# Kernel tuning notes

Measured on AMD Instinct MI355X. Metric: run time of the kernel, lower is better.

Reference implementation:

```python
import jax, jax.numpy as jnp
import numpy as np

B, N, M = 2, 2048, 2048
Q_DIM = 1024
HEADS = 8
DIM_HEAD = 64
INNER = HEADS * DIM_HEAD  # 512


def setup_inputs() -> dict:
    key = jax.random.key(0)
    ks = jax.random.split(key, 7)
    s_in = 1.0 / np.sqrt(Q_DIM)
    s_out = 1.0 / np.sqrt(INNER)
    return {
        "x": jax.random.normal(ks[0], (B, N, Q_DIM), dtype=jnp.float32),
        "context": jax.random.normal(ks[1], (B, M, Q_DIM), dtype=jnp.float32),
        "Wq": jax.random.normal(ks[2], (Q_DIM, INNER), dtype=jnp.float32) * s_in,
        "Wk": jax.random.normal(ks[3], (Q_DIM, INNER), dtype=jnp.float32) * s_in,
        "Wv": jax.random.normal(ks[4], (Q_DIM, INNER), dtype=jnp.float32) * s_in,
        "Wo": jax.random.normal(ks[5], (INNER, Q_DIM), dtype=jnp.float32) * s_out,
        "bo": jax.random.normal(ks[6], (Q_DIM,), dtype=jnp.float32) * 0.01,
    }


def reference(x, context, Wq, Wk, Wv, Wo, bo):
    scale = DIM_HEAD ** (-0.5)
    # projections, split heads: [b, n, inner] -> [b, h, n, d]
    def split_heads(t):
        b, n, _ = t.shape
        return t.reshape(b, n, HEADS, DIM_HEAD).transpose(0, 2, 1, 3)
    q = split_heads(x @ Wq)
    k = split_heads(context @ Wk)
    v = split_heads(context @ Wv)
    sim = jnp.einsum('bhid,bhjd->bhij', q, k) * scale  # [b,h,n,m] full score matrix
    attn = jax.nn.softmax(sim, axis=-1)
    out = jnp.einsum('bhij,bhjd->bhid', attn, v)       # [b,h,n,d]
    out = out.transpose(0, 2, 1, 3).reshape(x.shape[0], x.shape[1], INNER)
    return out @ Wo + bo
```

## Files before the change

kernel.cpp:

```cpp
#include <hip/hip_runtime.h>

typedef __attribute__((ext_vector_type(8))) short short8;
typedef __attribute__((ext_vector_type(4))) float floatx4;
typedef __attribute__((ext_vector_type(16))) float f32x16;
typedef __attribute__((ext_vector_type(4))) float f32x4;
typedef __attribute__((ext_vector_type(2))) unsigned uint2v;

__device__ __forceinline__ short f2bf(float f) {
    union { float f; unsigned u; } v;
    v.f = f;
    unsigned r = v.u + 0x7fffu + ((v.u >> 16) & 1u);
    return (short)(r >> 16);
}

#define MFMA_BF16(a, b, c) __builtin_amdgcn_mfma_f32_16x16x32_bf16((a), (b), (c), 0, 0, 0)
#define MFMA32(a, b, c)    __builtin_amdgcn_mfma_f32_32x32x16_bf16((a), (b), (c), 0, 0, 0)

__device__ __forceinline__ float fast_exp2(float x) {
#if __has_builtin(__builtin_amdgcn_exp2f)
    return __builtin_amdgcn_exp2f(x);
#else
    return exp2f(x);
#endif
}

__device__ __forceinline__ unsigned cvtpk(float lo, float hi) {
    unsigned r;
    asm("v_cvt_pk_bf16_f32 %0, %1, %2" : "=v"(r) : "v"(lo), "v"(hi));
    return r;
}

__device__ __forceinline__ void pl32(unsigned& a, unsigned& b) {
    asm("v_permlane32_swap_b32 %0, %1" : "+v"(a), "+v"(b));
}

__device__ __forceinline__ void gll16(const void* g, void* l) {
    __builtin_amdgcn_global_load_lds((const __attribute__((address_space(1))) void*)g,
                                     (__attribute__((address_space(3))) void*)l,
                                     16, 0, 0);
}

#define QSCALE_LOG2E 0.18033688011112042f

__global__ __launch_bounds__(256) void wfrag_all(const float* __restrict__ Wq,
                                                 const float* __restrict__ Wk,
                                                 const float* __restrict__ Wv,
                                                 const float* __restrict__ Wo,
                                                 short* __restrict__ WqF,
                                                 short* __restrict__ WkF,
                                                 short* __restrict__ WvF,
                                                 short* __restrict__ WoF) {
    const int z = blockIdx.y;
    const float* src = (z == 0) ? Wq : (z == 1) ? Wk : (z == 2) ? Wv : Wo;
    short* dst = (z == 0) ? WqF : (z == 1) ? WkF : (z == 2) ? WvF : WoF;
    const int nbits = (z < 3) ? 9 : 10;
    const int N = 1 << nbits;
    const int t = blockIdx.x * 256 + threadIdx.x;
    const int kb = t >> nbits;
    const int n = t & (N - 1);
    const float* s = src + (size_t)(kb * 8) * N + n;
    short8 v;
#pragma unroll
    for (int j = 0; j < 8; ++j) v[j] = f2bf(s[(size_t)j * N]);
    *(short8*)(dst + (size_t)t * 8) = v;
}

__global__ __launch_bounds__(256) void afrag(const float* __restrict__ x,
                                             const float* __restrict__ ctx,
                                             short* __restrict__ AxF,
                                             short* __restrict__ AcF) {
    const float* src = (blockIdx.z == 0) ? x : ctx;
    short* dst = (blockIdx.z == 0) ? AxF : AcF;
    const int r0 = blockIdx.x * 64;
    const int k0 = blockIdx.y * 64;
    __shared__ short tile[64][72];
    const int tid = threadIdx.x;
    {
        const int seg = tid & 15;
        const int rbase = tid >> 4;
#pragma unroll
        for (int i = 0; i < 4; ++i) {
            const int row = rbase + i * 16;
            f32x4 v = *(const f32x4*)(src + (size_t)(r0 + row) * 1024 + k0 + seg * 4);
            uint2v d;
            d[0] = cvtpk(v[0], v[1]);
            d[1] = cvtpk(v[2], v[3]);
            *(uint2v*)&tile[row][seg * 4] = d;
        }
    }
    __syncthreads();
    {
        const int kbl = tid >> 5;
        const int rbase = tid & 31;
#pragma unroll
        for (int j = 0; j < 2; ++j) {
            const int row = rbase + j * 32;
            short8 v = *(const short8*)(&tile[row][kbl * 8]);
            *(short8*)(dst + ((size_t)(k0 / 8 + kbl) * 4096 + r0 + row) * 8) = v;
        }
    }
}

__global__ __launch_bounds__(256) void gemm_qkv(const short* __restrict__ AxF,
                                                const short* __restrict__ AcF,
                                                const short* __restrict__ WqF,
                                                const short* __restrict__ WkF,
                                                const short* __restrict__ WvF,
                                                short* __restrict__ Qw,
                                                short* __restrict__ Kw,
                                                short* __restrict__ Vtw) {
    const int z = blockIdx.z;
    const short* AF = (z == 0) ? AxF : AcF;
    const short* WF = (z == 0) ? WqF : (z == 1) ? WkF : WvF;
    const int tid = threadIdx.x;
    const int w = tid >> 6;
    const int lane = tid & 63;
    const int quad = lane >> 4, ln = lane & 15;
    const int wr = w >> 1, wc = w & 1;
    const int row0 = blockIdx.x * 64;
    const int col0 = blockIdx.y * 128;

    __shared__ __align__(16) short lds[2][12288];

    auto stage = [&](int buf, int kt) {
        short* d = &lds[buf][0];
        const int kb0 = kt * 8;
#pragma unroll
        for (int c = 0; c < 2; ++c) {
            const int kb = c * 4 + w;
            gll16(AF + ((size_t)(kb0 + kb) * 4096 + row0 + lane) * 8,
                  d + kb * 512);
        }
#pragma unroll
        for (int c = 0; c < 4; ++c) {
            const int g = c * 4 + w;
            const int kb = g >> 1, colb = (g & 1) * 64;
            gll16(WF + ((size_t)(kb0 + kb) * 512 + col0 + colb + lane) * 8,
                  d + 4096 + (kb * 128 + colb) * 8);
        }
    };

    floatx4 acc[2][4] = {};

    auto compute = [&](int buf) {
        const short* sA = &lds[buf][0];
        const short* sB = &lds[buf][4096];
#pragma unroll
        for (int s = 0; s < 2; ++s) {
            const int kb = s * 4 + quad;
            short8 aF[2], bF[4];
#pragma unroll
            for (int i = 0; i < 2; ++i)
                aF[i] = *(const short8*)(sA + (kb * 64 + wr * 32 + i * 16 + ln) * 8);
#pragma unroll
            for (int j = 0; j < 4; ++j)
                bF[j] = *(const short8*)(sB + (kb * 128 + wc * 64 + j * 16 + ln) * 8);
#pragma unroll
            for (int i = 0; i < 2; ++i)
#pragma unroll
                for (int j = 0; j < 4; ++j)
                    acc[i][j] = MFMA_BF16(aF[i], bF[j], acc[i][j]);
        }
    };

    stage(0, 0);
    __syncthreads();
    for (int t = 0; t < 16; ++t) {
        if (t + 1 < 16) stage((t + 1) & 1, t + 1);
        compute(t & 1);
        __syncthreads();
    }

    const float oscale = (z == 0) ? QSCALE_LOG2E : 1.0f;
    short* dst = (z == 0) ? Qw : (z == 1) ? Kw : Vtw;
#pragma unroll
    for (int i = 0; i < 2; ++i)
#pragma unroll
        for (int t = 0; t < 4; ++t)
#pragma unroll
            for (int r = 0; r < 4; ++r) {
                const int R = row0 + wr * 32 + i * 16 + quad * 4 + r;
                const int C = col0 + wc * 64 + t * 16 + ln;
                const int b = R >> 11, n = R & 2047;
                const int h = C >> 6, d = C & 63;
                const short val = f2bf(acc[i][t][r] * oscale);
                if (z < 2)
                    dst[((b * 8 + h) * 2048 + n) * 64 + d] = val;
                else
                    dst[((b * 8 + h) * 64 + d) * 2048 + n] = val;
            }
}

__global__ __launch_bounds__(256, 2) void attn_kernel(const short* __restrict__ Q,
                                                      const short* __restrict__ K,
                                                      const short* __restrict__ Vt,
                                                      short* __restrict__ AwF) {
    const int tid = threadIdx.x;
    const int w = tid >> 6;
    const int lane = tid & 63;
    const int hi = lane >> 5;
    const int ln5 = lane & 31;

    const int L = blockIdx.x + 32 * blockIdx.y;
    const int xcd = L & 7, slot = L >> 3;
    const int bh = xcd * 2 + (slot >> 5);
    const int q0 = (slot & 31) * 64;

    __shared__ __align__(16) char smem[65536];
    char* const wbase = smem + w * 16384;

    const short* Qbh = Q + (size_t)bh * 2048 * 64;
    const char* kp = (const char*)(K + (size_t)bh * 2048 * 64);
    const char* vp = (const char*)(Vt + (size_t)bh * 64 * 2048);

    short8 qf[2][4];
#pragma unroll
    for (int qt = 0; qt < 2; ++qt)
#pragma unroll
        for (int ds = 0; ds < 4; ++ds)
            qf[qt][ds] = *(const short8*)(Qbh + (size_t)(q0 + qt * 32 + ln5) * 64 + ds * 16 + hi * 8);

    f32x16 O[2][2] = {};
    float lp0 = 0.f, lp1 = 0.f;

    const int lrow = lane >> 3, lu = lane & 7;
    const int swzK = ((lu ^ lrow) << 4);
    const int sw_r = (ln5 & 7) << 4;

    auto stageK = [&](int tile, int c) {
        char* kb = wbase + c * 8192;
#pragma unroll
        for (int i = 0; i < 4; ++i)
            gll16(kp + (size_t)tile * 4096 + (size_t)i * 1024 + lrow * 128 + swzK,
                  kb + i * 1024);
    };
    auto stageV = [&](int tile, int c) {
        char* vb = wbase + c * 8192 + 4096;
#pragma unroll
        for (int i = 0; i < 4; ++i) {
            const int u = lu ^ lrow;
            const int d = i * 8 + lrow + 32 * (u >> 2);
            gll16(vp + (size_t)d * 4096 + (size_t)tile * 64 + (u & 3) * 16,
                  vb + i * 1024);
        }
    };

    short8 PA[2][2];

    auto computeTile = [&](int c) {
        char* kb = wbase + c * 8192;
        char* vb = kb + 4096;
        short8 kf[4];
#pragma unroll
        for (int ds = 0; ds < 4; ++ds)
            kf[ds] = *(const short8*)(kb + ln5 * 128 + ((((ds * 2 + hi) << 4)) ^ sw_r));
        short8 vf[2][2];
#pragma unroll
        for (int dt = 0; dt < 2; ++dt)
#pragma unroll
            for (int k2 = 0; k2 < 2; ++k2)
                vf[dt][k2] = *(const short8*)(vb + ln5 * 128 +
                                              ((((dt * 4 + k2 * 2 + hi) << 4)) ^ sw_r));
        f32x16 s0 = {}, s1 = {};
        __builtin_amdgcn_s_setprio(1);
#pragma unroll
        for (int ds = 0; ds < 4; ++ds) {
            s0 = MFMA32(kf[ds], qf[0][ds], s0);
            s1 = MFMA32(kf[ds], qf[1][ds], s1);
        }
        __builtin_amdgcn_s_setprio(0);
        auto buildPA = [&](const f32x16& sv, float& lacc, short8& oA, short8& oB) {
            float p[16];
#pragma unroll
            for (int e = 0; e < 16; ++e) p[e] = fast_exp2(sv[e]);
            float t0 = 0.f, t1 = 0.f;
#pragma unroll
            for (int e = 0; e < 16; e += 2) { t0 += p[e]; t1 += p[e + 1]; }
            lacc += t0 + t1;
            unsigned c0 = cvtpk(p[0], p[1]),   c1 = cvtpk(p[2], p[3]);
            unsigned c2 = cvtpk(p[4], p[5]),   c3 = cvtpk(p[6], p[7]);
            unsigned c4 = cvtpk(p[8], p[9]),   c5 = cvtpk(p[10], p[11]);
            unsigned c6 = cvtpk(p[12], p[13]), c7 = cvtpk(p[14], p[15]);
            pl32(c0, c2); pl32(c1, c3);
            pl32(c4, c6); pl32(c5, c7);
            union U { short8 s8; unsigned u[4]; };
            U a; a.u[0] = c0; a.u[1] = c1; a.u[2] = c2; a.u[3] = c3; oA = a.s8;
            U b; b.u[0] = c4; b.u[1] = c5; b.u[2] = c6; b.u[3] = c7; oB = b.s8;
        };
        buildPA(s0, lp0, PA[0][0], PA[1][0]);
        buildPA(s1, lp1, PA[0][1], PA[1][1]);
        __builtin_amdgcn_s_setprio(1);
#pragma unroll
        for (int dt = 0; dt < 2; ++dt)
#pragma unroll
            for (int k2 = 0; k2 < 2; ++k2) {
                O[dt][0] = MFMA32(vf[dt][k2], PA[k2][0], O[dt][0]);
                O[dt][1] = MFMA32(vf[dt][k2], PA[k2][1], O[dt][1]);
            }
        __builtin_amdgcn_s_setprio(0);
    };

    stageK(w, 0);
    stageV(w, 0);
    int cur = 0;
    for (int t = 0; t < 16; ++t) {
        if (t < 15) {
            stageK(w + (t + 1) * 4, cur ^ 1);
            stageV(w + (t + 1) * 4, cur ^ 1);
            asm volatile("s_waitcnt vmcnt(8)" ::: "memory");
        } else {
            asm volatile("s_waitcnt vmcnt(0)" ::: "memory");
        }
        computeTile(cur);
        cur ^= 1;
    }
    __syncthreads();

    float* lpf = (float*)smem;
    {
        const float a = lp0 + __shfl_xor(lp0, 32);
        const float b = lp1 + __shfl_xor(lp1, 32);
        if (hi == 0) {
            lpf[w * 64 + ln5] = a;
            lpf[w * 64 + 32 + ln5] = b;
        }
    }
    __syncthreads();
    const int qq = tid & 63;
    const int k8a = tid >> 6;
    const float den = lpf[qq] + lpf[64 + qq] + lpf[128 + qq] + lpf[192 + qq];
    const float inv = 1.0f / den;
    __syncthreads();
    float* freg = (float*)smem + w * 4096;
#pragma unroll
    for (int dt = 0; dt < 2; ++dt)
#pragma unroll
        for (int qt = 0; qt < 2; ++qt)
#pragma unroll
            for (int e = 0; e < 16; ++e) {
                const int d = dt * 32 + (e & 3) + 8 * (e >> 2) + 4 * hi;
                freg[d * 64 + qt * 32 + ln5] = O[dt][qt][e];
            }
    __syncthreads();
    const int b = bh >> 3, h = bh & 7;
    const float* fall = (const float*)smem;
#pragma unroll
    for (int j = 0; j < 2; ++j) {
        const int k8 = k8a + j * 4;
        float a8[8];
#pragma unroll
        for (int dd = 0; dd < 8; ++dd) {
            const int d = k8 * 8 + dd;
            a8[dd] = fall[d * 64 + qq] + fall[4096 + d * 64 + qq] +
                     fall[8192 + d * 64 + qq] + fall[12288 + d * 64 + qq];
        }
        short8 o8;
#pragma unroll
        for (int dd = 0; dd < 8; ++dd) o8[dd] = f2bf(a8[dd] * inv);
        *(short8*)(AwF + ((size_t)(h * 8 + k8) * 4096 + (size_t)(b * 2048 + q0 + qq)) * 8) = o8;
    }
}

__global__ __launch_bounds__(256) void gemm_final(const short* __restrict__ AwF,
                                                  const short* __restrict__ WoF,
                                                  const float* __restrict__ bias,
                                                  float* __restrict__ out) {
    const int tid = threadIdx.x;
    const int w = tid >> 6;
    const int lane = tid & 63;
    const int quad = lane >> 4, ln = lane & 15;
    const int wr = w >> 1, wc = w & 1;
    const int row0 = blockIdx.x * 64;
    const int col0 = blockIdx.y * 128;

    __shared__ __align__(16) short lds[2][12288];

    auto stage = [&](int buf, int kt) {
        short* d = &lds[buf][0];
        const int kb0 = kt * 8;
#pragma unroll
        for (int c = 0; c < 2; ++c) {
            const int kb = c * 4 + w;
            gll16(AwF + ((size_t)(kb0 + kb) * 4096 + row0 + lane) * 8,
                  d + kb * 512);
        }
#pragma unroll
        for (int c = 0; c < 4; ++c) {
            const int g = c * 4 + w;
            const int kb = g >> 1, colb = (g & 1) * 64;
            gll16(WoF + ((size_t)(kb0 + kb) * 1024 + col0 + colb + lane) * 8,
                  d + 4096 + (kb * 128 + colb) * 8);
        }
    };

    floatx4 acc[2][4] = {};

    auto compute = [&](int buf) {
        const short* sA = &lds[buf][0];
        const short* sB = &lds[buf][4096];
#pragma unroll
        for (int s = 0; s < 2; ++s) {
            const int kb = s * 4 + quad;
            short8 aF[2], bF[4];
#pragma unroll
            for (int i = 0; i < 2; ++i)
                aF[i] = *(const short8*)(sA + (kb * 64 + wr * 32 + i * 16 + ln) * 8);
#pragma unroll
            for (int j = 0; j < 4; ++j)
                bF[j] = *(const short8*)(sB + (kb * 128 + wc * 64 + j * 16 + ln) * 8);
#pragma unroll
            for (int i = 0; i < 2; ++i)
#pragma unroll
                for (int j = 0; j < 4; ++j)
                    acc[i][j] = MFMA_BF16(aF[i], bF[j], acc[i][j]);
        }
    };

    stage(0, 0);
    __syncthreads();
    for (int t = 0; t < 8; ++t) {
        if (t + 1 < 8) stage((t + 1) & 1, t + 1);
        compute(t & 1);
        __syncthreads();
    }

#pragma unroll
    for (int i = 0; i < 2; ++i)
#pragma unroll
        for (int t = 0; t < 4; ++t)
#pragma unroll
            for (int r = 0; r < 4; ++r) {
                const int R = row0 + wr * 32 + i * 16 + quad * 4 + r;
                const int C = col0 + wc * 64 + t * 16 + ln;
                out[(size_t)R * 1024 + C] = acc[i][t][r] + bias[C];
            }
}

extern "C" void kernel_launch(void* const* d_in, const int* in_sizes, int n_in,
                              void* d_out, int out_size, void* d_ws, size_t ws_size,
                              hipStream_t stream) {
    const float* x   = (const float*)d_in[0];
    const float* ctx = (const float*)d_in[1];
    const float* Wq  = (const float*)d_in[2];
    const float* Wk  = (const float*)d_in[3];
    const float* Wv  = (const float*)d_in[4];
    const float* Wo  = (const float*)d_in[5];
    const float* bo  = (const float*)d_in[6];
    float* out = (float*)d_out;

    char* ws = (char*)d_ws;
    size_t off = 0;
    auto alloc = [&](size_t bytes) { char* p = ws + off; off += (bytes + 255) & ~(size_t)255; return p; };

    short* WqF  = (short*)alloc(512 * 1024 * 2);
    short* WkF  = (short*)alloc(512 * 1024 * 2);
    short* WvF  = (short*)alloc(512 * 1024 * 2);
    short* WoF  = (short*)alloc(1024 * 512 * 2);
    short* AxF  = (short*)alloc((size_t)4096 * 1024 * 2);
    short* AcF  = (short*)alloc((size_t)4096 * 1024 * 2);
    short* Qw   = (short*)alloc((size_t)16 * 2048 * 64 * 2);
    short* Kw   = (short*)alloc((size_t)16 * 2048 * 64 * 2);
    short* Vtw  = (short*)alloc((size_t)16 * 2048 * 64 * 2);
    short* AwF  = (short*)alloc((size_t)4096 * 512 * 2);

    wfrag_all<<<dim3(256, 4), 256, 0, stream>>>(Wq, Wk, Wv, Wo, WqF, WkF, WvF, WoF);
    afrag<<<dim3(64, 16, 2), 256, 0, stream>>>(x, ctx, AxF, AcF);

    gemm_qkv<<<dim3(64, 4, 3), 256, 0, stream>>>(AxF, AcF, WqF, WkF, WvF, Qw, Kw, Vtw);

    attn_kernel<<<dim3(32, 16), 256, 0, stream>>>(Qw, Kw, Vtw, AwF);

    gemm_final<<<dim3(64, 8), 256, 0, stream>>>(AwF, WoF, bo, out);
}
```

Measured before the change: 150.1 us.

## Stage V-transpose through LDS and double attention block query tile

The QKV GEMM epilogue for V now transposes the tile in shared memory and writes Vt with 16-byte vector stores instead of scattered 2-byte strided stores. The attention kernel moves to 512-thread blocks covering 128 queries: two query halves share the same per-wave K/V split, 128KB of LDS, and half as many blocks. This is meant to cut uncoalesced global writes and raise K/V reuse per block. In exchange it lowers block count (256 blocks at one per CU) and doubles the LDS footprint.

```diff
diff --git a/kernel.cpp b/kernel.cpp
--- a/kernel.cpp
+++ b/kernel.cpp
@@ -172,26 +172,47 @@
     }
 
     const float oscale = (z == 0) ? QSCALE_LOG2E : 1.0f;
-    short* dst = (z == 0) ? Qw : (z == 1) ? Kw : Vtw;
-#pragma unroll
-    for (int i = 0; i < 2; ++i)
-#pragma unroll
-        for (int t = 0; t < 4; ++t)
-#pragma unroll
-            for (int r = 0; r < 4; ++r) {
-                const int R = row0 + wr * 32 + i * 16 + quad * 4 + r;
-                const int C = col0 + wc * 64 + t * 16 + ln;
-                const int b = R >> 11, n = R & 2047;
-                const int h = C >> 6, d = C & 63;
-                const short val = f2bf(acc[i][t][r] * oscale);
-                if (z < 2)
-                    dst[((b * 8 + h) * 2048 + n) * 64 + d] = val;
-                else
-                    dst[((b * 8 + h) * 64 + d) * 2048 + n] = val;
-            }
-}
-
-__global__ __launch_bounds__(256, 2) void attn_kernel(const short* __restrict__ Q,
+    if (z < 2) {
+        short* dst = (z == 0) ? Qw : Kw;
+#pragma unroll
+        for (int i = 0; i < 2; ++i)
+#pragma unroll
+            for (int t = 0; t < 4; ++t)
+#pragma unroll
+                for (int r = 0; r < 4; ++r) {
+                    const int R = row0 + wr * 32 + i * 16 + quad * 4 + r;
+                    const int C = col0 + wc * 64 + t * 16 + ln;
+                    const int b = R >> 11, n = R & 2047;
+                    const int h = C >> 6, d = C & 63;
+                    dst[((b * 8 + h) * 2048 + n) * 64 + d] = f2bf(acc[i][t][r] * oscale);
+                }
+    } else {
+        short* t2 = (short*)&lds[0][0];
+#pragma unroll
+        for (int i = 0; i < 2; ++i)
+#pragma unroll
+            for (int t = 0; t < 4; ++t)
+#pragma unroll
+                for (int r = 0; r < 4; ++r) {
+                    const int lr = wr * 32 + i * 16 + quad * 4 + r;
+                    const int lc = wc * 64 + t * 16 + ln;
+                    t2[lc * 72 + lr] = f2bf(acc[i][t][r]);
+                }
+        __syncthreads();
+        const int c = tid >> 1, halfr = (tid & 1) * 32;
+        const int C = col0 + c;
+        const int h = C >> 6, d = C & 63;
+        const int b = row0 >> 11;
+        const int n0 = (row0 & 2047) + halfr;
+        short* gp = Vtw + (((size_t)(b * 8 + h) * 64 + d) * 2048) + n0;
+        const short* sp = t2 + c * 72 + halfr;
+#pragma unroll
+        for (int u = 0; u < 4; ++u)
+            *(short8*)(gp + u * 8) = *(const short8*)(sp + u * 8);
+    }
+}
+
+__global__ __launch_bounds__(512, 1) void attn_kernel(const short* __restrict__ Q,
                                                       const short* __restrict__ K,
                                                       const short* __restrict__ Vt,
                                                       short* __restrict__ AwF) {
@@ -200,25 +221,28 @@
     const int lane = tid & 63;
     const int hi = lane >> 5;
     const int ln5 = lane & 31;
-
-    const int L = blockIdx.x + 32 * blockIdx.y;
+    const int qh = w & 1;
+    const int kvr = w >> 1;
+
+    const int L = blockIdx.x + 16 * blockIdx.y;
     const int xcd = L & 7, slot = L >> 3;
-    const int bh = xcd * 2 + (slot >> 5);
-    const int q0 = (slot & 31) * 64;
-
-    __shared__ __align__(16) char smem[65536];
+    const int bh = xcd * 2 + (slot >> 4);
+    const int q0 = (slot & 15) * 128;
+
+    __shared__ __align__(16) char smem[131072];
     char* const wbase = smem + w * 16384;
 
     const short* Qbh = Q + (size_t)bh * 2048 * 64;
     const char* kp = (const char*)(K + (size_t)bh * 2048 * 64);
     const char* vp = (const char*)(Vt + (size_t)bh * 64 * 2048);
 
+    const int qbase = q0 + qh * 64;
     short8 qf[2][4];
 #pragma unroll
     for (int qt = 0; qt < 2; ++qt)
 #pragma unroll
         for (int ds = 0; ds < 4; ++ds)
-            qf[qt][ds] = *(const short8*)(Qbh + (size_t)(q0 + qt * 32 + ln5) * 64 + ds * 16 + hi * 8);
+            qf[qt][ds] = *(const short8*)(Qbh + (size_t)(qbase + qt * 32 + ln5) * 64 + ds * 16 + hi * 8);
 
     f32x16 O[2][2] = {};
     float lp0 = 0.f, lp1 = 0.f;
@@ -300,13 +324,13 @@
         __builtin_amdgcn_s_setprio(0);
     };
 
-    stageK(w, 0);
-    stageV(w, 0);
+    stageK(kvr, 0);
+    stageV(kvr, 0);
     int cur = 0;
     for (int t = 0; t < 16; ++t) {
         if (t < 15) {
-            stageK(w + (t + 1) * 4, cur ^ 1);
-            stageV(w + (t + 1) * 4, cur ^ 1);
+            stageK(kvr + (t + 1) * 4, cur ^ 1);
+            stageV(kvr + (t + 1) * 4, cur ^ 1);
             asm volatile("s_waitcnt vmcnt(8)" ::: "memory");
         } else {
             asm volatile("s_waitcnt vmcnt(0)" ::: "memory");
@@ -321,14 +345,16 @@
         const float a = lp0 + __shfl_xor(lp0, 32);
         const float b = lp1 + __shfl_xor(lp1, 32);
         if (hi == 0) {
-            lpf[w * 64 + ln5] = a;
-            lpf[w * 64 + 32 + ln5] = b;
-        }
-    }
-    __syncthreads();
-    const int qq = tid & 63;
-    const int k8a = tid >> 6;
-    const float den = lpf[qq] + lpf[64 + qq] + lpf[128 + qq] + lpf[192 + qq];
+            lpf[(qh * 4 + kvr) * 64 + ln5] = a;
+            lpf[(qh * 4 + kvr) * 64 + 32 + ln5] = b;
+        }
+    }
+    __syncthreads();
+    const int qq = tid & 127;
+    const int k8a = tid >> 7;
+    const int g = qq >> 6, qr = qq & 63;
+    const float den = lpf[(g * 4 + 0) * 64 + qr] + lpf[(g * 4 + 1) * 64 + qr] +
+                      lpf[(g * 4 + 2) * 64 + qr] + lpf[(g * 4 + 3) * 64 + qr];
     const float inv = 1.0f / den;
     __syncthreads();
     float* freg = (float*)smem + w * 4096;
@@ -351,8 +377,8 @@
 #pragma unroll
         for (int dd = 0; dd < 8; ++dd) {
             const int d = k8 * 8 + dd;
-            a8[dd] = fall[d * 64 + qq] + fall[4096 + d * 64 + qq] +
-                     fall[8192 + d * 64 + qq] + fall[12288 + d * 64 + qq];
+            a8[dd] = fall[(g + 0) * 4096 + d * 64 + qr] + fall[(g + 2) * 4096 + d * 64 + qr] +
+                     fall[(g + 4) * 4096 + d * 64 + qr] + fall[(g + 6) * 4096 + d * 64 + qr];
         }
         short8 o8;
 #pragma unroll
@@ -468,7 +494,7 @@
 
     gemm_qkv<<<dim3(64, 4, 3), 256, 0, stream>>>(AxF, AcF, WqF, WkF, WvF, Qw, Kw, Vtw);
 
-    attn_kernel<<<dim3(32, 16), 256, 0, stream>>>(Qw, Kw, Vtw, AwF);
+    attn_kernel<<<dim3(16, 16), 512, 0, stream>>>(Qw, Kw, Vtw, AwF);
 
     gemm_final<<<dim3(64, 8), 256, 0, stream>>>(AwF, WoF, bo, out);
 }
```

New measurement: 152.5 us. No clear change (+1.6%).

## Fuse fp32-to-bf16 activation conversion into QKV GEMM and stage V transpose via LDS

Applied to the files above, without the earlier changes.

Removes the separate afrag kernel and its intermediate bf16 fragment buffers. The QKV GEMM now reads fp32 x/context directly, converts to bf16 in registers and writes a padded row-major A tile into LDS, with loads for the next tile issued before compute. The V output is transposed through LDS so each thread writes contiguous 16-byte vectors instead of strided scalar stores. The cost is that each GEMM block reads fp32 A data, twice the bytes of the old bf16 fragments, and A is re-read across column blocks and the K/V z-slices. Converting in registers also adds VALU work to the GEMM loop.

```diff
diff --git a/kernel.cpp b/kernel.cpp
--- a/kernel.cpp
+++ b/kernel.cpp
@@ -65,44 +65,8 @@
     *(short8*)(dst + (size_t)t * 8) = v;
 }
 
-__global__ __launch_bounds__(256) void afrag(const float* __restrict__ x,
-                                             const float* __restrict__ ctx,
-                                             short* __restrict__ AxF,
-                                             short* __restrict__ AcF) {
-    const float* src = (blockIdx.z == 0) ? x : ctx;
-    short* dst = (blockIdx.z == 0) ? AxF : AcF;
-    const int r0 = blockIdx.x * 64;
-    const int k0 = blockIdx.y * 64;
-    __shared__ short tile[64][72];
-    const int tid = threadIdx.x;
-    {
-        const int seg = tid & 15;
-        const int rbase = tid >> 4;
-#pragma unroll
-        for (int i = 0; i < 4; ++i) {
-            const int row = rbase + i * 16;
-            f32x4 v = *(const f32x4*)(src + (size_t)(r0 + row) * 1024 + k0 + seg * 4);
-            uint2v d;
-            d[0] = cvtpk(v[0], v[1]);
-            d[1] = cvtpk(v[2], v[3]);
-            *(uint2v*)&tile[row][seg * 4] = d;
-        }
-    }
-    __syncthreads();
-    {
-        const int kbl = tid >> 5;
-        const int rbase = tid & 31;
-#pragma unroll
-        for (int j = 0; j < 2; ++j) {
-            const int row = rbase + j * 32;
-            short8 v = *(const short8*)(&tile[row][kbl * 8]);
-            *(short8*)(dst + ((size_t)(k0 / 8 + kbl) * 4096 + r0 + row) * 8) = v;
-        }
-    }
-}
-
-__global__ __launch_bounds__(256) void gemm_qkv(const short* __restrict__ AxF,
-                                                const short* __restrict__ AcF,
+__global__ __launch_bounds__(256) void gemm_qkv(const float* __restrict__ x,
+                                                const float* __restrict__ ctx,
                                                 const short* __restrict__ WqF,
                                                 const short* __restrict__ WkF,
                                                 const short* __restrict__ WvF,
@@ -110,7 +74,7 @@
                                                 short* __restrict__ Kw,
                                                 short* __restrict__ Vtw) {
     const int z = blockIdx.z;
-    const short* AF = (z == 0) ? AxF : AcF;
+    const float* As = (z == 0) ? x : ctx;
     const short* WF = (z == 0) ? WqF : (z == 1) ? WkF : WvF;
     const int tid = threadIdx.x;
     const int w = tid >> 6;
@@ -120,38 +84,52 @@
     const int row0 = blockIdx.x * 64;
     const int col0 = blockIdx.y * 128;
 
-    __shared__ __align__(16) short lds[2][12288];
-
-    auto stage = [&](int buf, int kt) {
-        short* d = &lds[buf][0];
+    __shared__ __align__(16) short lds[25600];
+    auto aP = [&](int buf) { return lds + buf * 4608; };
+    auto bP = [&](int buf) { return lds + 9216 + buf * 8192; };
+
+    const int seg = tid & 15;
+    const int rb = tid >> 4;
+
+    auto loadA = [&](int kt, f32x4* vn) {
+#pragma unroll
+        for (int i = 0; i < 4; ++i)
+            vn[i] = *(const f32x4*)(As + (size_t)(row0 + rb + i * 16) * 1024 + kt * 64 + seg * 4);
+    };
+    auto writeA = [&](int buf, const f32x4* vn) {
+        short* a = aP(buf);
+#pragma unroll
+        for (int i = 0; i < 4; ++i) {
+            uint2v d;
+            d[0] = cvtpk(vn[i][0], vn[i][1]);
+            d[1] = cvtpk(vn[i][2], vn[i][3]);
+            *(uint2v*)(a + (rb + i * 16) * 72 + seg * 4) = d;
+        }
+    };
+    auto stageB = [&](int buf, int kt) {
+        short* d = bP(buf);
         const int kb0 = kt * 8;
-#pragma unroll
-        for (int c = 0; c < 2; ++c) {
-            const int kb = c * 4 + w;
-            gll16(AF + ((size_t)(kb0 + kb) * 4096 + row0 + lane) * 8,
-                  d + kb * 512);
-        }
 #pragma unroll
         for (int c = 0; c < 4; ++c) {
             const int g = c * 4 + w;
             const int kb = g >> 1, colb = (g & 1) * 64;
             gll16(WF + ((size_t)(kb0 + kb) * 512 + col0 + colb + lane) * 8,
-                  d + 4096 + (kb * 128 + colb) * 8);
+                  d + (kb * 128 + colb) * 8);
         }
     };
 
     floatx4 acc[2][4] = {};
 
     auto compute = [&](int buf) {
-        const short* sA = &lds[buf][0];
-        const short* sB = &lds[buf][4096];
+        const short* sA = aP(buf);
+        const short* sB = bP(buf);
 #pragma unroll
         for (int s = 0; s < 2; ++s) {
             const int kb = s * 4 + quad;
             short8 aF[2], bF[4];
 #pragma unroll
             for (int i = 0; i < 2; ++i)
-                aF[i] = *(const short8*)(sA + (kb * 64 + wr * 32 + i * 16 + ln) * 8);
+                aF[i] = *(const short8*)(sA + (wr * 32 + i * 16 + ln) * 72 + kb * 8);
 #pragma unroll
             for (int j = 0; j < 4; ++j)
                 bF[j] = *(const short8*)(sB + (kb * 128 + wc * 64 + j * 16 + ln) * 8);
@@ -163,32 +141,66 @@
         }
     };
 
-    stage(0, 0);
-    __syncthreads();
+    {
+        f32x4 v0[4];
+        loadA(0, v0);
+        stageB(0, 0);
+        writeA(0, v0);
+    }
+    __syncthreads();
+    int cur = 0;
     for (int t = 0; t < 16; ++t) {
-        if (t + 1 < 16) stage((t + 1) & 1, t + 1);
-        compute(t & 1);
+        f32x4 vn[4];
+        const bool more = (t + 1 < 16);
+        if (more) {
+            loadA(t + 1, vn);
+            stageB(cur ^ 1, t + 1);
+        }
+        compute(cur);
+        if (more) writeA(cur ^ 1, vn);
         __syncthreads();
+        cur ^= 1;
     }
 
     const float oscale = (z == 0) ? QSCALE_LOG2E : 1.0f;
-    short* dst = (z == 0) ? Qw : (z == 1) ? Kw : Vtw;
-#pragma unroll
-    for (int i = 0; i < 2; ++i)
-#pragma unroll
-        for (int t = 0; t < 4; ++t)
-#pragma unroll
-            for (int r = 0; r < 4; ++r) {
-                const int R = row0 + wr * 32 + i * 16 + quad * 4 + r;
-                const int C = col0 + wc * 64 + t * 16 + ln;
-                const int b = R >> 11, n = R & 2047;
-                const int h = C >> 6, d = C & 63;
-                const short val = f2bf(acc[i][t][r] * oscale);
-                if (z < 2)
-                    dst[((b * 8 + h) * 2048 + n) * 64 + d] = val;
-                else
-                    dst[((b * 8 + h) * 64 + d) * 2048 + n] = val;
-            }
+    if (z < 2) {
+        short* dst = (z == 0) ? Qw : Kw;
+#pragma unroll
+        for (int i = 0; i < 2; ++i)
+#pragma unroll
+            for (int t = 0; t < 4; ++t)
+#pragma unroll
+                for (int r = 0; r < 4; ++r) {
+                    const int R = row0 + wr * 32 + i * 16 + quad * 4 + r;
+                    const int C = col0 + wc * 64 + t * 16 + ln;
+                    const int b = R >> 11, n = R & 2047;
+                    const int h = C >> 6, d = C & 63;
+                    dst[((b * 8 + h) * 2048 + n) * 64 + d] = f2bf(acc[i][t][r] * oscale);
+                }
+    } else {
+        short* t2 = lds;
+#pragma unroll
+        for (int i = 0; i < 2; ++i)
+#pragma unroll
+            for (int t = 0; t < 4; ++t)
+#pragma unroll
+                for (int r = 0; r < 4; ++r) {
+                    const int lr = wr * 32 + i * 16 + quad * 4 + r;
+                    const int lc = wc * 64 + t * 16 + ln;
+                    t2[lc * 72 + lr] = f2bf(acc[i][t][r]);
+                }
+        __syncthreads();
+        const int c = tid >> 1, halfr = (tid & 1) * 32;
+        const int C = col0 + c;
+        const int h = C >> 6, d = C & 63;
+        const int b = row0 >> 11;
+        const int n0 = (row0 & 2047) + halfr;
+        short* gp = Vtw + (((size_t)(b * 8 + h) * 64 + d) * 2048) + n0;
+        const short* sp = t2 + c * 72 + halfr;
+#pragma unroll
+        for (int u = 0; u < 4; ++u)
+            *(short8*)(gp + u * 8) = *(const short8*)(sp + u * 8);
+    }
 }
 
 __global__ __launch_bounds__(256, 2) void attn_kernel(const short* __restrict__ Q,
@@ -456,17 +468,14 @@
     short* WkF  = (short*)alloc(512 * 1024 * 2);
     short* WvF  = (short*)alloc(512 * 1024 * 2);
     short* WoF  = (short*)alloc(1024 * 512 * 2);
-    short* AxF  = (short*)alloc((size_t)4096 * 1024 * 2);
-    short* AcF  = (short*)alloc((size_t)4096 * 1024 * 2);
     short* Qw   = (short*)alloc((size_t)16 * 2048 * 64 * 2);
     short* Kw   = (short*)alloc((size_t)16 * 2048 * 64 * 2);
     short* Vtw  = (short*)alloc((size_t)16 * 2048 * 64 * 2);
     short* AwF  = (short*)alloc((size_t)4096 * 512 * 2);
 
     wfrag_all<<<dim3(256, 4), 256, 0, stream>>>(Wq, Wk, Wv, Wo, WqF, WkF, WvF, WoF);
-    afrag<<<dim3(64, 16, 2), 256, 0, stream>>>(x, ctx, AxF, AcF);
-
-    gemm_qkv<<<dim3(64, 4, 3), 256, 0, stream>>>(AxF, AcF, WqF, WkF, WvF, Qw, Kw, Vtw);
+
+    gemm_qkv<<<dim3(64, 4, 3), 256, 0, stream>>>(x, ctx, WqF, WkF, WvF, Qw, Kw, Vtw);
 
     attn_kernel<<<dim3(32, 16), 256, 0, stream>>>(Qw, Kw, Vtw, AwF);
 
```

After: 150.1 us (median of 2 runs). Within noise of the previous version (+0.0%).
